# Optimization experiments

Measured on AMD Instinct MI355X. Metric: run time of the kernel, lower is better.

Reference implementation:

```python
import jax, jax.numpy as jnp
import numpy as np
import math

B, T, D = 8, 1024, 1024
N, L = 256, 768
H = 16
TE = 2048  # time_embed_dim
EPS = 1e-5


def _ln(x, g, b):
    mu = jnp.mean(x, axis=-1, keepdims=True)
    var = jnp.mean(jnp.square(x - mu), axis=-1, keepdims=True)
    return (x - mu) * jax.lax.rsqrt(var + EPS) * g + b


def setup_inputs() -> dict:
    key = jax.random.key(0)
    ks = jax.random.split(key, 16)
    s = lambda fan_in: 1.0 / math.sqrt(fan_in)
    return {
        "x": jax.random.normal(ks[0], (B, T, D), jnp.float32),
        "xf": jax.random.normal(ks[1], (B, N, L), jnp.float32),
        "emb": jax.random.normal(ks[2], (B, TE), jnp.float32),
        "ln_g": jnp.ones((D,), jnp.float32),
        "ln_b": jnp.zeros((D,), jnp.float32),
        "cln_g": jnp.ones((L,), jnp.float32),
        "cln_b": jnp.zeros((L,), jnp.float32),
        "Wq": jax.random.normal(ks[3], (D, D), jnp.float32) * s(D),
        "bq": jnp.zeros((D,), jnp.float32),
        "Wk": jax.random.normal(ks[4], (L, D), jnp.float32) * s(L),
        "bk": jnp.zeros((D,), jnp.float32),
        "Wv": jax.random.normal(ks[5], (L, D), jnp.float32) * s(L),
        "bv": jnp.zeros((D,), jnp.float32),
        "sln_g": jnp.ones((D,), jnp.float32),
        "sln_b": jnp.zeros((D,), jnp.float32),
        "Wemb": jax.random.normal(ks[6], (TE, 2 * D), jnp.float32) * s(TE),
        "bemb": jnp.zeros((2 * D,), jnp.float32),
        "Wout": jax.random.normal(ks[7], (D, D), jnp.float32) * s(D) * 0.02,
        "bout": jnp.zeros((D,), jnp.float32),
    }


def reference(x, xf, emb, ln_g, ln_b, cln_g, cln_b, Wq, bq, Wk, bk, Wv, bv,
              sln_g, sln_b, Wemb, bemb, Wout, bout):
    # x: (B,T,D), xf: (B,N,L), emb: (B,TE)
    hd = D // H
    q = (_ln(x, ln_g, ln_b) @ Wq + bq).reshape(B, T, H, hd)
    xf_n = _ln(xf, cln_g, cln_b)
    k = (xf_n @ Wk + bk).reshape(B, N, H, hd)
    v = (xf_n @ Wv + bv).reshape(B, N, H, hd)
    # scores: (B,T,N,H); note: scaled by sqrt(D//H)
    att = jnp.einsum('bthd,bnhd->btnh', q, k) / math.sqrt(hd)
    w = jax.nn.softmax(att, axis=2)  # softmax over conditioning tokens N
    y = jnp.einsum('btnh,bnhd->bthd', w, v).reshape(B, T, D)
    # StylizationBlock (dropout = 0)
    emb_out = jax.nn.silu(emb) @ Wemb + bemb  # (B, 2D)
    scale, shift = jnp.split(emb_out[:, None, :], 2, axis=2)
    h = _ln(y, sln_g, sln_b) * (1.0 + scale) + shift
    h = jax.nn.silu(h) @ Wout + bout
    return x + h
```

## Files before the change

kernel.cpp:

```cpp
#include <hip/hip_runtime.h>
#include <hip/hip_bf16.h>

typedef __hip_bfloat16 bf16;
typedef unsigned short ushort;
typedef unsigned char uchar;
typedef long i64;
typedef __attribute__((ext_vector_type(4))) float f32x4;

#define B_ 8
#define T_ 1024
#define D_ 1024
#define N_ 256
#define L_ 768
#define H_ 16
#define HD_ 64
#define TE_ 2048

__device__ __forceinline__ void gld16(const void* g, void* l) {
    __builtin_amdgcn_global_load_lds((const __attribute__((address_space(1))) void*)g,
                                     (__attribute__((address_space(3))) void*)l,
                                     16, 0, 0);
}

__device__ __forceinline__ float bitf(unsigned u) { return __uint_as_float(u); }

__device__ __forceinline__ int pk4_fp8(float a, float b, float c, float d) {
    int p = __builtin_amdgcn_cvt_pk_fp8_f32(a, b, 0, false);
    p = __builtin_amdgcn_cvt_pk_fp8_f32(c, d, p, true);
    return p;
}
__device__ __forceinline__ uchar pk1_fp8(float a) {
    int p = __builtin_amdgcn_cvt_pk_fp8_f32(a, a, 0, false);
    return (uchar)(p & 0xff);
}
__device__ __forceinline__ float dec8(uchar b) {
    int e = (b >> 3) & 15, m = b & 7;
    float mag = e ? (float)(8 + m) * bitf((unsigned)(117 + e) << 23)
                  : (float)m * bitf(118u << 23);
    return (b & 0x80) ? -mag : mag;
}

template <int NV>
__device__ __forceinline__ void ln_row(const float* __restrict__ rp,
                                       const float* __restrict__ g,
                                       const float* __restrict__ bb,
                                       uchar* __restrict__ op, int lane) {
    float4 va[NV];
#pragma unroll
    for (int i = 0; i < NV; i++) va[i] = ((const float4*)rp)[i * 64 + lane];
    float s = 0.f, s2 = 0.f;
#pragma unroll
    for (int i = 0; i < NV; i++) {
        s  += va[i].x + va[i].y + va[i].z + va[i].w;
        s2 += va[i].x * va[i].x + va[i].y * va[i].y + va[i].z * va[i].z + va[i].w * va[i].w;
    }
#pragma unroll
    for (int off = 32; off; off >>= 1) {
        s  += __shfl_xor(s,  off, 64);
        s2 += __shfl_xor(s2, off, 64);
    }
    const float inv_n = 1.f / (float)(NV * 256);
    float mu = s * inv_n;
    float var = s2 * inv_n - mu * mu;
    float rstd = rsqrtf(var + 1e-5f);
#pragma unroll
    for (int i = 0; i < NV; i++) {
        float4 gv = ((const float4*)g)[i * 64 + lane];
        float4 bv = ((const float4*)bb)[i * 64 + lane];
        ((int*)op)[i * 64 + lane] = pk4_fp8((va[i].x - mu) * rstd * gv.x + bv.x,
                                            (va[i].y - mu) * rstd * gv.y + bv.y,
                                            (va[i].z - mu) * rstd * gv.z + bv.z,
                                            (va[i].w - mu) * rstd * gv.w + bv.w);
    }
}

__global__ __launch_bounds__(256) void prep_kernel(
        const float* __restrict__ x, const float* __restrict__ xf,
        const float* __restrict__ g1, const float* __restrict__ b1,
        const float* __restrict__ g2, const float* __restrict__ b2,
        const float* __restrict__ Wq, const float* __restrict__ Wk,
        const float* __restrict__ Wv, const float* __restrict__ Wo,
        const float* __restrict__ emb, const float* __restrict__ Wemb,
        uchar* __restrict__ xn8, uchar* __restrict__ xfn8,
        uchar* __restrict__ wq8, uchar* __restrict__ wk8,
        uchar* __restrict__ wv8, uchar* __restrict__ wo8,
        float* __restrict__ part) {
    __shared__ __align__(16) char smem[16384];
    int bid = blockIdx.x;
    int tid = threadIdx.x;
    if (bid < 2560) {
        int w = tid >> 6, lane = tid & 63;
        int row = bid * 4 + w;
        if (row < B_ * T_) {
            ln_row<4>(x + (size_t)row * D_, g1, b1, xn8 + (size_t)row * D_, lane);
        } else {
            int r = row - B_ * T_;
            ln_row<3>(xf + (size_t)r * L_, g2, b2, xfn8 + (size_t)r * L_, lane);
        }
    } else if (bid < 3456) {
        uchar (*t)[65] = (uchar(*)[65])smem;
        int id = bid - 2560;
        int xb = id & 15, y = id >> 4;
        const float* W; uchar* Wt; int K, ky;
        if (y < 16)      { W = Wq; Wt = wq8; K = 1024; ky = y; }
        else if (y < 28) { W = Wk; Wt = wk8; K = 768;  ky = y - 16; }
        else if (y < 40) { W = Wv; Wt = wv8; K = 768;  ky = y - 28; }
        else             { W = Wo; Wt = wo8; K = 1024; ky = y - 40; }
        int k0 = ky * 64, n0 = xb * 64;
#pragma unroll
        for (int i = 0; i < 16; i++) {
            int e = tid + i * 256;
            int r = e >> 6, c = e & 63;
            t[r][c] = pk1_fp8(W[(size_t)(k0 + r) * D_ + n0 + c]);
        }
        __syncthreads();
#pragma unroll
        for (int i = 0; i < 4; i++) {
            int e = tid + i * 256;
            int r = e >> 4, cg = (e & 15) * 4;
            unsigned u = (unsigned)t[cg][r] | ((unsigned)t[cg + 1][r] << 8)
                       | ((unsigned)t[cg + 2][r] << 16) | ((unsigned)t[cg + 3][r] << 24);
            *(unsigned*)&Wt[(size_t)(n0 + r) * K + k0 + cg] = u;
        }
    } else {
        float* se  = (float*)smem;
        float* red = (float*)(smem + 8192);
        int id = bid - 3456;
        int j0 = (id & 31) * 64;
        int ks = id >> 5;
        int tx = tid & 15, ty = tid >> 4;
        int w = tid >> 6, lane = tid & 63;
#pragma unroll
        for (int b = 0; b < 8; b++) {
            float xv = emb[b * TE_ + ks * 256 + tid];
            se[b * 256 + tid] = xv / (1.f + __expf(-xv));
        }
        __syncthreads();
        float acc[8][4] = {};
#pragma unroll 4
        for (int i = 0; i < 16; i++) {
            int e = ty + 16 * i;
            float4 wv = *(const float4*)&Wemb[(size_t)(ks * 256 + e) * 2048 + j0 + tx * 4];
#pragma unroll
            for (int b = 0; b < 8; b++) {
                float s = se[b * 256 + e];
                acc[b][0] += s * wv.x; acc[b][1] += s * wv.y;
                acc[b][2] += s * wv.z; acc[b][3] += s * wv.w;
            }
        }
#pragma unroll
        for (int b = 0; b < 8; b++)
#pragma unroll
            for (int m = 0; m < 4; m++) {
                float v = acc[b][m];
                v += __shfl_down(v, 32, 64);
                v += __shfl_down(v, 16, 64);
                if (lane < 16) red[(w * 8 + b) * 64 + lane * 4 + m] = v;
            }
        __syncthreads();
        for (int o = tid; o < 512; o += 256) {
            int b = o >> 6, jl = o & 63;
            float s = red[(0 * 8 + b) * 64 + jl] + red[(1 * 8 + b) * 64 + jl]
                    + red[(2 * 8 + b) * 64 + jl] + red[(3 * 8 + b) * 64 + jl];
            part[((size_t)ks * 8 + b) * 2048 + j0 + jl] = s;
        }
    }
}

template <int MODE>
__device__ __forceinline__ void gemm_body(const uchar* __restrict__ Ap,
                                          const uchar* __restrict__ Bp,
                                          const float* __restrict__ bias,
                                          const float* __restrict__ res,
                                          void* __restrict__ Cout,
                                          int m0, int n0, int Ncols, int K,
                                          uchar* SH) {
    int tid = threadIdx.x;
    int w = tid >> 6, lane = tid & 63;
    int quad = lane >> 4, l15 = lane & 15;
    int wm = (w >> 1) * 64, wn = (w & 1) * 64;
    int lr4 = lane >> 2;
    int sp4 = lane & 3;
    uchar* A0 = SH;
    uchar* B0 = SH + 8192;
    uchar* A1 = SH + 16384;
    uchar* B1 = SH + 24576;
    f32x4 acc[4][4] = {};

    auto stage = [&](int kt, uchar* As, uchar* Bs) {
#pragma unroll
        for (int j = 0; j < 2; j++) {
            int r = w * 32 + j * 16 + lr4;
            int gc = sp4 ^ (r & 3);
            gld16(&Ap[(size_t)(m0 + r) * K + kt + gc * 16], &As[(w * 32 + j * 16) * 64]);
        }
#pragma unroll
        for (int j = 0; j < 2; j++) {
            int r = w * 32 + j * 16 + lr4;
            int gc = sp4 ^ (r & 3);
            gld16(&Bp[(size_t)(n0 + r) * K + kt + gc * 16], &Bs[(w * 32 + j * 16) * 64]);
        }
    };
    auto compute = [&](const uchar* As, const uchar* Bs) {
#pragma unroll
        for (int kh = 0; kh < 2; kh++) {
            int c4 = kh * 2 + (quad >> 1);
            int sub = (quad & 1) * 8;
            int pos = (c4 ^ (l15 & 3)) * 16 + sub;
            i64 af[4], bfr[4];
#pragma unroll
            for (int mt = 0; mt < 4; mt++)
                af[mt] = *(const i64*)&As[(wm + mt * 16 + l15) * 64 + pos];
#pragma unroll
            for (int nt = 0; nt < 4; nt++)
                bfr[nt] = *(const i64*)&Bs[(wn + nt * 16 + l15) * 64 + pos];
#pragma unroll
            for (int mt = 0; mt < 4; mt++)
#pragma unroll
                for (int nt = 0; nt < 4; nt++)
                    acc[mt][nt] = __builtin_amdgcn_mfma_f32_16x16x32_fp8_fp8(af[mt], bfr[nt], acc[mt][nt], 0, 0, 0);
        }
    };

    int nt2 = K >> 6;
    stage(0, A0, B0);
    __syncthreads();
    for (int t = 0; t + 2 <= nt2; t += 2) {
        stage((t + 1) * 64, A1, B1);
        compute(A0, B0);
        __syncthreads();
        if (t + 2 < nt2) stage((t + 2) * 64, A0, B0);
        compute(A1, B1);
        __syncthreads();
    }

    if (MODE == 0) {
#pragma unroll
        for (int mt = 0; mt < 4; mt++)
#pragma unroll
            for (int nt = 0; nt < 4; nt++)
#pragma unroll
                for (int reg = 0; reg < 4; reg++) {
                    int rl = wm + mt * 16 + quad * 4 + reg;
                    int cl = wn + nt * 16 + l15;
                    SH[rl * 128 + cl] = pk1_fp8(acc[mt][nt][reg] + bias[n0 + cl]);
                }
        __syncthreads();
#pragma unroll
        for (int i = 0; i < 4; i++) {
            int row = (tid >> 3) + i * 32;
            int ch = (tid & 7) * 16;
            *(int4*)&((uchar*)Cout)[(size_t)(m0 + row) * Ncols + n0 + ch] =
                *(const int4*)&SH[row * 128 + ch];
        }
    } else {
#pragma unroll
        for (int mt = 0; mt < 4; mt++) {
#pragma unroll
            for (int nt = 0; nt < 4; nt++) {
#pragma unroll
                for (int reg = 0; reg < 4; reg++) {
                    int row = m0 + wm + mt * 16 + quad * 4 + reg;
                    int col = n0 + wn + nt * 16 + l15;
                    float v = acc[mt][nt][reg] + bias[col];
                    if (MODE == 1) {
                        v += res[(size_t)row * Ncols + col];
                        ((float*)Cout)[(size_t)row * Ncols + col] = v;
                    } else {
                        int b = row >> 8, n = row & 255;
                        int h = col >> 6, d = col & 63;
                        size_t addr = ((size_t)(b * 16 + h)) * 16384 + (size_t)d * 256
                                    + (((n >> 4) ^ (d & 15)) * 16) + (n & 15);
                        ((uchar*)Cout)[addr] = pk1_fp8(v);
                    }
                }
            }
        }
    }
}

__global__ __launch_bounds__(256, 4) void qkv_gemm(const uchar* __restrict__ xn8,
                                                   const uchar* __restrict__ xfn8,
                                                   const uchar* __restrict__ wq8,
                                                   const uchar* __restrict__ wk8,
                                                   const uchar* __restrict__ wv8,
                                                   const float* __restrict__ bq,
                                                   const float* __restrict__ bk,
                                                   const float* __restrict__ bv,
                                                   uchar* __restrict__ q8,
                                                   uchar* __restrict__ k8,
                                                   uchar* __restrict__ vT8,
                                                   const float* __restrict__ part,
                                                   const float* __restrict__ bemb,
                                                   float* __restrict__ embo) {
    __shared__ __align__(16) uchar SH[32768];
    int bid = blockIdx.x;
    if (bid < 512) {
        gemm_body<0>(xn8, wq8, bq, nullptr, q8,
                     (bid & 63) * 128, (bid >> 6) * 128, D_, D_, SH);
    } else if (bid < 640) {
        int id = bid - 512;
        gemm_body<0>(xfn8, wk8, bk, nullptr, k8,
                     (id & 15) * 128, (id >> 4) * 128, D_, L_, SH);
    } else if (bid < 768) {
        int id = bid - 640;
        gemm_body<2>(xfn8, wv8, bv, nullptr, vT8,
                     (id & 15) * 128, (id >> 4) * 128, D_, L_, SH);
    } else {
        int o = (bid - 768) * 256 + threadIdx.x;
        int b = o >> 11, j = o & 2047;
        float s = bemb[j];
#pragma unroll
        for (int ks = 0; ks < 8; ks++) s += part[((size_t)ks * 8 + b) * 2048 + j];
        embo[o] = s;
    }
}

__global__ __launch_bounds__(256, 4) void out_gemm(const uchar* __restrict__ a8,
                                                   const uchar* __restrict__ wo8,
                                                   const float* __restrict__ bout,
                                                   const float* __restrict__ x,
                                                   float* __restrict__ out) {
    __shared__ __align__(16) uchar SH[32768];
    int bid = blockIdx.x;
    gemm_body<1>(a8, wo8, bout, x, out,
                 (bid & 63) * 128, (bid >> 6) * 128, D_, D_, SH);
}

__global__ __launch_bounds__(256) void attn_mfma(const uchar* __restrict__ q8,
                                                 const uchar* __restrict__ k8,
                                                 const uchar* __restrict__ vT8,
                                                 uchar* __restrict__ y8) {
    __shared__ __align__(16) uchar KV[16384];
    __shared__ __align__(16) uchar P[8192];
    int tid = threadIdx.x;
    int w = tid >> 6, lane = tid & 63;
    int quad = lane >> 4, l15 = lane & 15;
    int bid = blockIdx.x;
    int work = (bid & 7) * 256 + (bid >> 3);
    int t0 = (work & 15) * 64;
    int bh = work >> 4;
    int b = bh >> 4, h = bh & 15;
    int lln = lane >> 3, sp = lane & 7;

#pragma unroll
    for (int j = 0; j < 4; j++) {
        int dn = w * 32 + j * 8 + lln;
        int c8 = sp ^ (dn & 7);
        int n = dn * 2 + (c8 >> 2);
        gld16(&k8[(size_t)(b * N_ + n) * D_ + h * 64 + (c8 & 3) * 16],
              &KV[(w * 32 + j * 8) * 128]);
    }
#pragma unroll
    for (int j = 0; j < 2; j++) {
        int r = w * 16 + j * 8 + lln;
        int c = (sp ^ (r & 7)) & 3;
        gld16(&q8[(size_t)(b * T_ + t0 + r) * D_ + h * 64 + c * 16],
              &P[(w * 16 + j * 8) * 128]);
    }
    __syncthreads();

    int qrow = w * 16 + l15;
    i64 aq0, aq1;
    {
        int c0 = (quad >> 1);
        int c1 = 2 + (quad >> 1);
        aq0 = *(const i64*)&P[qrow * 128 + ((c0 ^ (qrow & 7)) * 16) + (quad & 1) * 8];
        aq1 = *(const i64*)&P[qrow * 128 + ((c1 ^ (qrow & 7)) * 16) + (quad & 1) * 8];
    }

    f32x4 sf[16];
#pragma unroll
    for (int nt = 0; nt < 16; nt++) {
        int n = nt * 16 + l15;
        int dn = n >> 1, hn = n & 1;
        int c80 = (hn * 4 + 0 + (quad >> 1)) ^ (dn & 7);
        int c81 = (hn * 4 + 2 + (quad >> 1)) ^ (dn & 7);
        i64 b0 = *(const i64*)&KV[dn * 128 + c80 * 16 + (quad & 1) * 8];
        i64 b1 = *(const i64*)&KV[dn * 128 + c81 * 16 + (quad & 1) * 8];
        f32x4 z = {};
        f32x4 t = __builtin_amdgcn_mfma_f32_16x16x32_fp8_fp8(b0, aq0, z, 0, 0, 0);
        sf[nt] = __builtin_amdgcn_mfma_f32_16x16x32_fp8_fp8(b1, aq1, t, 0, 0, 0);
    }
    __syncthreads();

    const uchar* vbase = vT8 + (size_t)(b * 16 + h) * 16384;
#pragma unroll
    for (int j = 0; j < 4; j++) {
        gld16(&vbase[(w * 4 + j) * 1024 + lane * 16], &KV[(w * 4 + j) * 1024]);
    }

    const float scale = 0.125f;
    float sm = 0.f;
#pragma unroll
    for (int nt = 0; nt < 16; nt++)
#pragma unroll
        for (int reg = 0; reg < 4; reg++) {
            float e = __expf(sf[nt][reg] * scale);
            sf[nt][reg] = e;
            sm += e;
        }
    sm += __shfl_xor(sm, 16, 64);
    sm += __shfl_xor(sm, 32, 64);
    float inv = 1.f / sm;
    __syncthreads();

    f32x4 of[4] = {};
    int srcLo = 32 * (quad & 1) + l15;
#pragma unroll
    for (int kk = 0; kk < 8; kk++) {
        int pkA = pk4_fp8(sf[2 * kk][0], sf[2 * kk][1], sf[2 * kk][2], sf[2 * kk][3]);
        int pkB = pk4_fp8(sf[2 * kk + 1][0], sf[2 * kk + 1][1], sf[2 * kk + 1][2], sf[2 * kk + 1][3]);
        int loA = __shfl(pkA, srcLo, 64);
        int hiA = __shfl(pkA, srcLo + 16, 64);
        int loB = __shfl(pkB, srcLo, 64);
        int hiB = __shfl(pkB, srcLo + 16, 64);
        unsigned lo = (quad >> 1) ? (unsigned)loB : (unsigned)loA;
        unsigned hi = (quad >> 1) ? (unsigned)hiB : (unsigned)hiA;
        i64 pf = (i64)(((unsigned long long)hi << 32) | (unsigned long long)lo);
        int ck = kk * 2 + (quad >> 1);
#pragma unroll
        for (int dt = 0; dt < 4; dt++) {
            int d = dt * 16 + l15;
            i64 bv = *(const i64*)&KV[d * 256 + ((ck ^ (d & 15)) * 16) + (quad & 1) * 8];
            of[dt] = __builtin_amdgcn_mfma_f32_16x16x32_fp8_fp8(bv, pf, of[dt], 0, 0, 0);
        }
    }

#pragma unroll
    for (int dt = 0; dt < 4; dt++) {
        int ov = pk4_fp8(of[dt][0] * inv, of[dt][1] * inv, of[dt][2] * inv, of[dt][3] * inv);
        *(int*)&P[qrow * 64 + ((dt ^ (l15 & 3)) * 16) + quad * 4] = ov;
    }
    __syncthreads();
    {
        int row = tid >> 2, c = tid & 3;
        *(int4*)&y8[(size_t)(b * T_ + t0 + row) * D_ + h * 64 + c * 16] =
            *(const int4*)&P[row * 64 + ((c ^ (row & 3)) * 16)];
    }
}

__global__ __launch_bounds__(256) void styl_kernel(const uchar* __restrict__ y8,
                                                   const float* __restrict__ g,
                                                   const float* __restrict__ bb,
                                                   const float* __restrict__ embo,
                                                   uchar* __restrict__ a8) {
    int tid = threadIdx.x, w = tid >> 6, lane = tid & 63;
    int row = blockIdx.x * 4 + w;
    int b = row >> 10;
    const uchar* rp = y8 + (size_t)row * D_;
    uchar* op = a8 + (size_t)row * D_;
    float v[16];
    float s = 0.f, s2 = 0.f;
#pragma unroll
    for (int i = 0; i < 4; i++) {
        unsigned u = ((const unsigned*)rp)[i * 64 + lane];
#pragma unroll
        for (int j = 0; j < 4; j++) {
            float f = dec8((uchar)(u >> (8 * j)));
            v[i * 4 + j] = f; s += f; s2 += f * f;
        }
    }
#pragma unroll
    for (int off = 32; off; off >>= 1) {
        s  += __shfl_xor(s,  off, 64);
        s2 += __shfl_xor(s2, off, 64);
    }
    float mu = s * (1.f / 1024.f);
    float rstd = rsqrtf(s2 * (1.f / 1024.f) - mu * mu + 1e-5f);
#pragma unroll
    for (int i = 0; i < 4; i++) {
        int c4 = i * 64 + lane;
        float4 gv  = ((const float4*)g)[c4];
        float4 bv  = ((const float4*)bb)[c4];
        float4 scv = ((const float4*)(embo + b * 2048))[c4];
        float4 shv = ((const float4*)(embo + b * 2048 + 1024))[c4];
        float h0 = (v[i*4+0] - mu) * rstd * gv.x + bv.x;
        float h1 = (v[i*4+1] - mu) * rstd * gv.y + bv.y;
        float h2 = (v[i*4+2] - mu) * rstd * gv.z + bv.z;
        float h3 = (v[i*4+3] - mu) * rstd * gv.w + bv.w;
        h0 = h0 * (1.f + scv.x) + shv.x;
        h1 = h1 * (1.f + scv.y) + shv.y;
        h2 = h2 * (1.f + scv.z) + shv.z;
        h3 = h3 * (1.f + scv.w) + shv.w;
        h0 = h0 / (1.f + __expf(-h0));
        h1 = h1 / (1.f + __expf(-h1));
        h2 = h2 / (1.f + __expf(-h2));
        h3 = h3 / (1.f + __expf(-h3));
        ((int*)op)[c4] = pk4_fp8(h0, h1, h2, h3);
    }
}

extern "C" void kernel_launch(void* const* d_in, const int* in_sizes, int n_in,
                              void* d_out, int out_size, void* d_ws, size_t ws_size,
                              hipStream_t stream) {
    const float* x    = (const float*)d_in[0];
    const float* xf   = (const float*)d_in[1];
    const float* emb  = (const float*)d_in[2];
    const float* ln_g = (const float*)d_in[3];
    const float* ln_b = (const float*)d_in[4];
    const float* cln_g= (const float*)d_in[5];
    const float* cln_b= (const float*)d_in[6];
    const float* Wq   = (const float*)d_in[7];
    const float* bq   = (const float*)d_in[8];
    const float* Wk   = (const float*)d_in[9];
    const float* bk   = (const float*)d_in[10];
    const float* Wv   = (const float*)d_in[11];
    const float* bv   = (const float*)d_in[12];
    const float* sln_g= (const float*)d_in[13];
    const float* sln_b= (const float*)d_in[14];
    const float* Wemb = (const float*)d_in[15];
    const float* bemb = (const float*)d_in[16];
    const float* Wout = (const float*)d_in[17];
    const float* bout = (const float*)d_in[18];
    float* out = (float*)d_out;

    char* wsp = (char*)d_ws;
    const size_t MB = 1024 * 1024;
    uchar* xn8  = (uchar*)(wsp);
    uchar* xfn8 = (uchar*)(wsp + 8 * MB);
    uchar* wq8  = (uchar*)(wsp + 10 * MB);
    uchar* wk8  = (uchar*)(wsp + 11 * MB);
    uchar* wv8  = (uchar*)(wsp + 12 * MB);
    uchar* wo8  = (uchar*)(wsp + 13 * MB);
    uchar* q8   = (uchar*)(wsp + 14 * MB);
    uchar* k8   = (uchar*)(wsp + 22 * MB);
    uchar* vT8  = (uchar*)(wsp + 24 * MB);
    uchar* y8   = (uchar*)(wsp + 26 * MB);
    uchar* a8   = (uchar*)(wsp + 34 * MB);
    float* embo = (float*)(wsp + 42 * MB);
    float* part = (float*)(wsp + 43 * MB);

    prep_kernel<<<3712, 256, 0, stream>>>(x, xf, ln_g, ln_b, cln_g, cln_b,
                                          Wq, Wk, Wv, Wout, emb, Wemb,
                                          xn8, xfn8, wq8, wk8, wv8, wo8, part);

    qkv_gemm<<<832, 256, 0, stream>>>(xn8, xfn8, wq8, wk8, wv8, bq, bk, bv,
                                      q8, k8, vT8, part, bemb, embo);

    attn_mfma<<<2048, 256, 0, stream>>>(q8, k8, vT8, y8);

    styl_kernel<<<2048, 256, 0, stream>>>(y8, sln_g, sln_b, embo, a8);

    out_gemm<<<512, 256, 0, stream>>>(a8, wo8, bout, x, out);
}
```

Before: 229.7 us.

## Triple-buffer FP8 GEMM k-loop with partial vmcnt waits and raw barriers

Replaces the double-buffered GEMM main loop with a three-stage LDS ring, so two tiles are in flight while one is computed. Each step waits only for the older group of global-to-LDS loads (vmcnt(4)) and uses a raw s_barrier instead of the full __syncthreads drain. This is meant to hide global load latency behind MFMA work. LDS per block grows from 32 KB to 48 KB, which may limit the four-blocks-per-CU occupancy target. Reusing a buffer one step after it was read relies on the single barrier per step for correctness.

```diff
diff --git a/kernel.cpp b/kernel.cpp
--- a/kernel.cpp
+++ b/kernel.cpp
@@ -181,10 +181,9 @@
     int wm = (w >> 1) * 64, wn = (w & 1) * 64;
     int lr4 = lane >> 2;
     int sp4 = lane & 3;
-    uchar* A0 = SH;
-    uchar* B0 = SH + 8192;
-    uchar* A1 = SH + 16384;
-    uchar* B1 = SH + 24576;
+    uchar* A0 = SH;              uchar* B0 = SH + 8192;
+    uchar* A1 = SH + 16384;      uchar* B1 = SH + 24576;
+    uchar* A2 = SH + 32768;      uchar* B2 = SH + 40960;
     f32x4 acc[4][4] = {};
 
     auto stage = [&](int kt, uchar* As, uchar* Bs) {
@@ -221,17 +220,28 @@
                     acc[mt][nt] = __builtin_amdgcn_mfma_f32_16x16x32_fp8_fp8(af[mt], bfr[nt], acc[mt][nt], 0, 0, 0);
         }
     };
-
     int nt2 = K >> 6;
+    auto step = [&](int tc, uchar* Ac, uchar* Bc, int tn, uchar* An, uchar* Bn) {
+        if (tc >= nt2) return;
+        if (tn < nt2) stage(tn * 64, An, Bn);
+        compute(Ac, Bc);
+        __builtin_amdgcn_sched_barrier(0);
+        if (tn < nt2) asm volatile("s_waitcnt vmcnt(4)" ::: "memory");
+        else          asm volatile("s_waitcnt vmcnt(0)" ::: "memory");
+        __builtin_amdgcn_s_barrier();
+        __builtin_amdgcn_sched_barrier(0);
+    };
+
     stage(0, A0, B0);
-    __syncthreads();
-    for (int t = 0; t + 2 <= nt2; t += 2) {
-        stage((t + 1) * 64, A1, B1);
-        compute(A0, B0);
-        __syncthreads();
-        if (t + 2 < nt2) stage((t + 2) * 64, A0, B0);
-        compute(A1, B1);
-        __syncthreads();
+    stage(64, A1, B1);
+    asm volatile("s_waitcnt vmcnt(4)" ::: "memory");
+    __builtin_amdgcn_s_barrier();
+    __builtin_amdgcn_sched_barrier(0);
+#pragma unroll 1
+    for (int t = 0; t < nt2; t += 3) {
+        step(t + 0, A0, B0, t + 2, A2, B2);
+        step(t + 1, A1, B1, t + 3, A0, B0);
+        step(t + 2, A2, B2, t + 4, A1, B1);
     }
 
     if (MODE == 0) {
@@ -293,7 +303,7 @@
                                                    const float* __restrict__ part,
                                                    const float* __restrict__ bemb,
                                                    float* __restrict__ embo) {
-    __shared__ __align__(16) uchar SH[32768];
+    __shared__ __align__(16) uchar SH[49152];
     int bid = blockIdx.x;
     if (bid < 512) {
         gemm_body<0>(xn8, wq8, bq, nullptr, q8,
@@ -321,7 +331,7 @@
                                                    const float* __restrict__ bout,
                                                    const float* __restrict__ x,
                                                    float* __restrict__ out) {
-    __shared__ __align__(16) uchar SH[32768];
+    __shared__ __align__(16) uchar SH[49152];
     int bid = blockIdx.x;
     gemm_body<1>(a8, wo8, bout, x, out,
                  (bid & 63) * 128, (bid >> 6) * 128, D_, D_, SH);
```

After: 246.3 us. 1.07x slower.
